# Kernel optimization log

Hardware: AMD Instinct MI355X
Metric: run time of the kernel (lower is better)

The kernel has to match this reference:

```python
import jax, jax.numpy as jnp
import numpy as np

N_NODES = 100000
N_EDGES = 640000
IN_CH, HID_CH, OUT_CH = 128, 256, 64


def setup_inputs() -> dict:
    key = jax.random.key(0)
    ks = jax.random.split(key, 6)
    x = jax.random.normal(ks[0], (N_NODES, IN_CH), dtype=jnp.float32)
    edge_index = jax.random.randint(ks[1], (2, N_EDGES), 0, N_NODES, dtype=jnp.int64)
    # Glorot-ish scaled weights
    W1l = jax.random.normal(ks[2], (HID_CH, IN_CH), dtype=jnp.float32) * (1.0 / np.sqrt(IN_CH))
    W1r = jax.random.normal(ks[3], (HID_CH, IN_CH), dtype=jnp.float32) * (1.0 / np.sqrt(IN_CH))
    W2l = jax.random.normal(ks[4], (OUT_CH, HID_CH), dtype=jnp.float32) * (1.0 / np.sqrt(HID_CH))
    W2r = jax.random.normal(ks[5], (OUT_CH, HID_CH), dtype=jnp.float32) * (1.0 / np.sqrt(HID_CH))
    b1 = jnp.zeros((HID_CH,), dtype=jnp.float32)
    b2 = jnp.zeros((OUT_CH,), dtype=jnp.float32)
    return {"x": x, "edge_index": edge_index, "W1l": W1l, "b1": b1, "W1r": W1r,
            "W2l": W2l, "b2": b2, "W2r": W2r}


def _sage_conv(x, src, dst, Wl, bl, Wr, n_nodes):
    # mean aggregation of source features at destination nodes (PyG aggr='mean')
    agg = jax.ops.segment_sum(x[src], dst, num_segments=n_nodes)          # [N, d]
    cnt = jax.ops.segment_sum(jnp.ones((src.shape[0], 1), x.dtype), dst,
                              num_segments=n_nodes)                        # [N, 1]
    mean = agg / jnp.maximum(cnt, 1.0)
    # out = lin_l(mean_neighbors) + lin_r(x); bias lives on lin_l
    return mean @ Wl.T + bl + x @ Wr.T


def reference(x, edge_index, W1l, b1, W1r, W2l, b2, W2r):
    src, dst = edge_index[0], edge_index[1]
    n = x.shape[0]
    h = _sage_conv(x, src, dst, W1l, b1, W1r, n)
    h = jax.nn.relu(h)
    out = _sage_conv(h, src, dst, W2l, b2, W2r, n)
    return out
```

## Files before the change

kernel.cpp:

```cpp
#include <hip/hip_runtime.h>


#define IN_CH  128
#define HID_CH 256
#define OUT_CH 64

typedef __bf16 bf16x8 __attribute__((ext_vector_type(8)));
typedef __bf16 bf16x4 __attribute__((ext_vector_type(4)));
typedef float  f32x4  __attribute__((ext_vector_type(4)));


__global__ void hist_kernel(const int* __restrict__ dst, int* __restrict__ deg, int E) {
    for (int e = blockIdx.x * blockDim.x + threadIdx.x; e < E; e += gridDim.x * blockDim.x)
        atomicAdd(&deg[dst[e]], 1);
}

__global__ void scan_block(const int* __restrict__ deg, int* __restrict__ offs,
                           int* __restrict__ bsum, int n) {
    __shared__ int s[512];
    int i = blockIdx.x * 512 + threadIdx.x;
    int v = (i < n) ? deg[i] : 0;
    s[threadIdx.x] = v;
    __syncthreads();
    #pragma unroll
    for (int d = 1; d < 512; d <<= 1) {
        int t = (threadIdx.x >= d) ? s[threadIdx.x - d] : 0;
        __syncthreads();
        s[threadIdx.x] += t;
        __syncthreads();
    }
    if (i < n) offs[i] = s[threadIdx.x] - v;
    if (threadIdx.x == 511) bsum[blockIdx.x] = s[511];
}

__global__ void scan_sums(int* __restrict__ bsum, int nb) {
    __shared__ int s[256];
    int v = (threadIdx.x < nb) ? bsum[threadIdx.x] : 0;
    s[threadIdx.x] = v;
    __syncthreads();
    #pragma unroll
    for (int d = 1; d < 256; d <<= 1) {
        int t = (threadIdx.x >= d) ? s[threadIdx.x - d] : 0;
        __syncthreads();
        s[threadIdx.x] += t;
        __syncthreads();
    }
    if (threadIdx.x < nb) bsum[threadIdx.x] = s[threadIdx.x] - v;
}

__global__ void scan_add(int* __restrict__ offs, const int* __restrict__ bsum, int n, int E) {
    int i = blockIdx.x * blockDim.x + threadIdx.x;
    if (i < n) offs[i] += bsum[i >> 9];
    if (i == 0) offs[n] = E;
}

__global__ void fill_csr(const int* __restrict__ src, const int* __restrict__ dst,
                         const int* __restrict__ offs, int* __restrict__ cur,
                         int* __restrict__ srcs, int E) {
    for (int e = blockIdx.x * blockDim.x + threadIdx.x; e < E; e += gridDim.x * blockDim.x) {
        int d = dst[e];
        int p = atomicAdd(&cur[d], 1);
        srcs[offs[d] + p] = src[e];
    }
}


__global__ void convert_weights(const float* __restrict__ W1l, const float* __restrict__ W1r,
                                const float* __restrict__ W2l, const float* __restrict__ W2r,
                                const float* __restrict__ b2,
                                __bf16* __restrict__ W1h, __bf16* __restrict__ W1lo,
                                __bf16* __restrict__ W2h, __bf16* __restrict__ W2lo,
                                float* __restrict__ bias2) {
    int i = blockIdx.x * 256 + threadIdx.x;
    if (i < 256 * 256) {
        int n = i >> 8, k = i & 255;
        float v = (k < 128) ? W1l[n * 128 + k] : W1r[n * 128 + (k - 128)];
        __bf16 h = (__bf16)v;
        W1h[i] = h; W1lo[i] = (__bf16)(v - (float)h);
    }
    if (i < 128 * 256) {
        int n = i >> 8, k = i & 255;
        float v = (n < 64) ? W2l[n * 256 + k] : W2r[(n - 64) * 256 + k];
        __bf16 h = (__bf16)v;
        W2h[i] = h; W2lo[i] = (__bf16)(v - (float)h);
    }
    if (i < 128) bias2[i] = (i < 64) ? 0.f : b2[i - 64];
}


__global__ __launch_bounds__(256) void agg_mean128(
    const float* __restrict__ X, const int* __restrict__ offs,
    const int* __restrict__ srcs, float* __restrict__ outm, int N) {
    int wv = (blockIdx.x * 256 + threadIdx.x) >> 6;
    int lane = threadIdx.x & 63;
    int grp = lane >> 5, l = lane & 31;
    int node = wv * 2 + grp;
    if (node >= N) return;
    int s0 = offs[node], s1 = offs[node + 1];
    float ax = 0.f, ay = 0.f, az = 0.f, aw = 0.f;
    int k = s0;
    for (; k + 4 <= s1; k += 4) {
        int i0 = srcs[k], i1 = srcs[k + 1], i2 = srcs[k + 2], i3 = srcs[k + 3];
        float4 a = *(const float4*)(X + (size_t)i0 * 128 + l * 4);
        float4 b = *(const float4*)(X + (size_t)i1 * 128 + l * 4);
        float4 c = *(const float4*)(X + (size_t)i2 * 128 + l * 4);
        float4 d = *(const float4*)(X + (size_t)i3 * 128 + l * 4);
        ax += (a.x + b.x) + (c.x + d.x);
        ay += (a.y + b.y) + (c.y + d.y);
        az += (a.z + b.z) + (c.z + d.z);
        aw += (a.w + b.w) + (c.w + d.w);
    }
    for (; k < s1; ++k) {
        int s = srcs[k];
        float4 a = *(const float4*)(X + (size_t)s * 128 + l * 4);
        ax += a.x; ay += a.y; az += a.z; aw += a.w;
    }
    int c = s1 - s0;
    float sc = 1.0f / (float)(c > 1 ? c : 1);
    float4 r; r.x = ax * sc; r.y = ay * sc; r.z = az * sc; r.w = aw * sc;
    *(float4*)(outm + (size_t)node * 128 + l * 4) = r;
}

__global__ __launch_bounds__(256) void agg_add_out(
    const float* __restrict__ Y2Z, const int* __restrict__ offs,
    const int* __restrict__ srcs, float* __restrict__ out, int N) {
    int wv = (blockIdx.x * 256 + threadIdx.x) >> 6;
    int lane = threadIdx.x & 63;
    int grp = lane >> 4, l = lane & 15;
    int node = wv * 4 + grp;
    if (node >= N) return;
    int s0 = offs[node], s1 = offs[node + 1];
    float4 z = *(const float4*)(Y2Z + (size_t)node * 128 + 64 + l * 4);
    float ax = 0.f, ay = 0.f, az = 0.f, aw = 0.f;
    int k = s0;
    for (; k + 4 <= s1; k += 4) {
        int i0 = srcs[k], i1 = srcs[k + 1], i2 = srcs[k + 2], i3 = srcs[k + 3];
        float4 a = *(const float4*)(Y2Z + (size_t)i0 * 128 + l * 4);
        float4 b = *(const float4*)(Y2Z + (size_t)i1 * 128 + l * 4);
        float4 c = *(const float4*)(Y2Z + (size_t)i2 * 128 + l * 4);
        float4 d = *(const float4*)(Y2Z + (size_t)i3 * 128 + l * 4);
        ax += (a.x + b.x) + (c.x + d.x);
        ay += (a.y + b.y) + (c.y + d.y);
        az += (a.z + b.z) + (c.z + d.z);
        aw += (a.w + b.w) + (c.w + d.w);
    }
    for (; k < s1; ++k) {
        int s = srcs[k];
        float4 a = *(const float4*)(Y2Z + (size_t)s * 128 + l * 4);
        ax += a.x; ay += a.y; az += a.z; aw += a.w;
    }
    int c = s1 - s0;
    float sc = 1.0f / (float)(c > 1 ? c : 1);
    float4 r;
    r.x = ax * sc + z.x; r.y = ay * sc + z.y;
    r.z = az * sc + z.z; r.w = aw * sc + z.w;
    *(float4*)(out + (size_t)node * 64 + l * 4) = r;
}


template<bool RELU>
__global__ __launch_bounds__(256) void gemm_split(
    const float* __restrict__ A1, int lda1,
    const float* __restrict__ A2, int lda2, int Ksplit,
    const __bf16* __restrict__ Whi, const __bf16* __restrict__ Wlo,
    const float* __restrict__ bias, float* __restrict__ C,
    int M, int K, int NT) {
    __shared__ __bf16 Ah[128 * 32], Al[128 * 32], Bh[128 * 32], Bl[128 * 32];
    const int tid = threadIdx.x;
    const int lane = tid & 63;
    const int wid = tid >> 6;
    const int wm = wid >> 1, wn = wid & 1;
    const int l15 = lane & 15, lg = lane >> 4;
    const long row0 = (long)blockIdx.x * 128;
    const int col0 = blockIdx.y * 128;

    const int ar  = tid >> 3;
    const int acx = (tid & 7) * 4;
    const int wrr = tid >> 2;
    const int wcx = (tid & 3) * 8;

    f32x4 acc[4][4] = {};

    for (int k0 = 0; k0 < K; k0 += 32) {
        const float* Asrc; int lda, kk0;
        if (k0 < Ksplit) { Asrc = A1; lda = lda1; kk0 = k0; }
        else             { Asrc = A2; lda = lda2; kk0 = k0 - Ksplit; }

        #pragma unroll
        for (int p = 0; p < 4; ++p) {
            int r = ar + p * 32;
            long gr = row0 + r;
            float4 v = make_float4(0.f, 0.f, 0.f, 0.f);
            if (gr < M) v = *(const float4*)(Asrc + gr * (long)lda + kk0 + acx);
            __bf16 h0 = (__bf16)v.x, h1 = (__bf16)v.y, h2 = (__bf16)v.z, h3 = (__bf16)v.w;
            bf16x4 hv, lv;
            hv[0] = h0; hv[1] = h1; hv[2] = h2; hv[3] = h3;
            lv[0] = (__bf16)(v.x - (float)h0); lv[1] = (__bf16)(v.y - (float)h1);
            lv[2] = (__bf16)(v.z - (float)h2); lv[3] = (__bf16)(v.w - (float)h3);
            int off = (r * 64 + acx * 2) ^ (((r >> 1) & 3) << 4);
            *(bf16x4*)((char*)Ah + off) = hv;
            *(bf16x4*)((char*)Al + off) = lv;
        }
        #pragma unroll
        for (int p = 0; p < 2; ++p) {
            int n = wrr + p * 64;
            long wrow = (long)(col0 + n) * K + k0 + wcx;
            bf16x8 hv = *(const bf16x8*)(Whi + wrow);
            bf16x8 lv = *(const bf16x8*)(Wlo + wrow);
            int off = (n * 64 + wcx * 2) ^ (((n >> 1) & 3) << 4);
            *(bf16x8*)((char*)Bh + off) = hv;
            *(bf16x8*)((char*)Bl + off) = lv;
        }
        __syncthreads();

        bf16x8 ah[4], al[4], bh[4], bl[4];
        #pragma unroll
        for (int m = 0; m < 4; ++m) {
            int r = wm * 64 + m * 16 + l15;
            int off = (r * 64 + lg * 16) ^ (((r >> 1) & 3) << 4);
            ah[m] = *(const bf16x8*)((char*)Ah + off);
            al[m] = *(const bf16x8*)((char*)Al + off);
        }
        #pragma unroll
        for (int n = 0; n < 4; ++n) {
            int r = wn * 64 + n * 16 + l15;
            int off = (r * 64 + lg * 16) ^ (((r >> 1) & 3) << 4);
            bh[n] = *(const bf16x8*)((char*)Bh + off);
            bl[n] = *(const bf16x8*)((char*)Bl + off);
        }
        #pragma unroll
        for (int m = 0; m < 4; ++m)
            #pragma unroll
            for (int n = 0; n < 4; ++n) {
                acc[m][n] = __builtin_amdgcn_mfma_f32_16x16x32_bf16(ah[m], bh[n], acc[m][n], 0, 0, 0);
                acc[m][n] = __builtin_amdgcn_mfma_f32_16x16x32_bf16(ah[m], bl[n], acc[m][n], 0, 0, 0);
                acc[m][n] = __builtin_amdgcn_mfma_f32_16x16x32_bf16(al[m], bh[n], acc[m][n], 0, 0, 0);
            }
        __syncthreads();
    }

    float bvals[4];
    #pragma unroll
    for (int n = 0; n < 4; ++n) bvals[n] = bias[col0 + wn * 64 + n * 16 + l15];
    #pragma unroll
    for (int m = 0; m < 4; ++m) {
        long gr0 = row0 + wm * 64 + m * 16 + lg * 4;
        #pragma unroll
        for (int rr = 0; rr < 4; ++rr) {
            long gr = gr0 + rr;
            if (gr < M) {
                #pragma unroll
                for (int n = 0; n < 4; ++n) {
                    int gc = col0 + wn * 64 + n * 16 + l15;
                    float v = acc[m][n][rr] + bvals[n];
                    if (RELU) v = fmaxf(v, 0.f);
                    C[gr * NT + gc] = v;
                }
            }
        }
    }
}


extern "C" void kernel_launch(void* const* d_in, const int* in_sizes, int n_in,
                              void* d_out, int out_size, void* d_ws, size_t ws_size,
                              hipStream_t stream) {
    const float* x   = (const float*)d_in[0];
    const int*   ei  = (const int*)d_in[1];
    const float* W1l = (const float*)d_in[2];
    const float* b1  = (const float*)d_in[3];
    const float* W1r = (const float*)d_in[4];
    const float* W2l = (const float*)d_in[5];
    const float* b2  = (const float*)d_in[6];
    const float* W2r = (const float*)d_in[7];
    float* out = (float*)d_out;

    const int N = in_sizes[0] / IN_CH;
    const int E = in_sizes[1] / 2;
    const int* src = ei;
    const int* dst = ei + E;

    float* h   = (float*)d_ws;
    float* buf = h + (size_t)N * HID_CH;
    int* deg  = (int*)(buf + (size_t)N * 128);
    int* offs = deg + N;
    int* cur  = offs + (N + 8);
    int* bsum = cur + N;
    int* srcs = bsum + 512;
    uintptr_t pp = (uintptr_t)(srcs + E);
    pp = (pp + 15) & ~(uintptr_t)15;
    __bf16* W1h  = (__bf16*)pp;
    __bf16* W1lo = W1h + 256 * 256;
    __bf16* W2h  = W1lo + 256 * 256;
    __bf16* W2lo = W2h + 128 * 256;
    float* bias2 = (float*)(W2lo + 128 * 256);

    hipMemsetAsync(deg, 0, sizeof(int) * N, stream);
    hipMemsetAsync(cur, 0, sizeof(int) * N, stream);

    convert_weights<<<256, 256, 0, stream>>>(W1l, W1r, W2l, W2r, b2,
                                             W1h, W1lo, W2h, W2lo, bias2);

    hist_kernel<<<1024, 256, 0, stream>>>(dst, deg, E);
    int nb = (N + 511) / 512;
    scan_block<<<nb, 512, 0, stream>>>(deg, offs, bsum, N);
    scan_sums<<<1, 256, 0, stream>>>(bsum, nb);
    scan_add<<<(N + 255) / 256, 256, 0, stream>>>(offs, bsum, N, E);
    fill_csr<<<1024, 256, 0, stream>>>(src, dst, offs, cur, srcs, E);

    agg_mean128<<<((N + 1) / 2 * 64 + 255) / 256, 256, 0, stream>>>(x, offs, srcs, buf, N);
    dim3 g1((N + 127) / 128, 2);
    gemm_split<true><<<g1, 256, 0, stream>>>(buf, IN_CH, x, IN_CH, IN_CH,
                                             W1h, W1lo, b1, h, N, 2 * IN_CH, HID_CH);

    dim3 g2((N + 127) / 128, 1);
    gemm_split<false><<<g2, 256, 0, stream>>>(nullptr, 0, h, HID_CH, 0,
                                              W2h, W2lo, bias2, buf, N, HID_CH, 2 * OUT_CH);
    agg_add_out<<<((N + 3) / 4 * 64 + 255) / 256, 256, 0, stream>>>(buf, offs, srcs, out, N);
}
```

Baseline: 376.6 us.

## Fuse layer-1 and layer-2 GEMMs keeping hidden activations in LDS

Replaces the two split-bf16 GEMM launches with one kernel that computes a 64-row tile of the layer-1 output (bias and ReLU applied), stores it as hi/lo bf16 in shared memory, and then multiplies it by the layer-2 weights. This removes the write and re-read of the N x 256 fp32 hidden tensor through global memory and drops one launch. In exchange each block uses 80 KB of LDS with 64-row tiles, which lowers occupancy and halves per-block row reuse of the weight tiles.

```diff
diff --git a/kernel.cpp b/kernel.cpp
--- a/kernel.cpp
+++ b/kernel.cpp
@@ -158,75 +158,73 @@
 }
 
 
-template<bool RELU>
-__global__ __launch_bounds__(256) void gemm_split(
-    const float* __restrict__ A1, int lda1,
-    const float* __restrict__ A2, int lda2, int Ksplit,
-    const __bf16* __restrict__ Whi, const __bf16* __restrict__ Wlo,
-    const float* __restrict__ bias, float* __restrict__ C,
-    int M, int K, int NT) {
-    __shared__ __bf16 Ah[128 * 32], Al[128 * 32], Bh[128 * 32], Bl[128 * 32];
+__global__ __launch_bounds__(256) void fused_l1l2(
+    const float* __restrict__ mean1, const float* __restrict__ x,
+    const __bf16* __restrict__ W1h, const __bf16* __restrict__ W1lo,
+    const float* __restrict__ b1,
+    const __bf16* __restrict__ W2h, const __bf16* __restrict__ W2lo,
+    const float* __restrict__ bias2,
+    float* __restrict__ Y2Z, int N) {
+    __shared__ __align__(16) char lds[80 * 1024];
+    __bf16* Hh    = (__bf16*)lds;
+    __bf16* Hl    = (__bf16*)(lds + 32 * 1024);
+    __bf16* W2hs  = (__bf16*)(lds + 64 * 1024);
+    __bf16* W2ls  = (__bf16*)(lds + 72 * 1024);
+    __bf16* Ah    = (__bf16*)lds;
+    __bf16* Al    = (__bf16*)(lds + 4 * 1024);
+    __bf16* B1h   = (__bf16*)(lds + 8 * 1024);
+    __bf16* B1l   = (__bf16*)(lds + 24 * 1024);
+
     const int tid = threadIdx.x;
     const int lane = tid & 63;
-    const int wid = tid >> 6;
-    const int wm = wid >> 1, wn = wid & 1;
+    const int w = tid >> 6;
     const int l15 = lane & 15, lg = lane >> 4;
-    const long row0 = (long)blockIdx.x * 128;
-    const int col0 = blockIdx.y * 128;
-
-    const int ar  = tid >> 3;
-    const int acx = (tid & 7) * 4;
-    const int wrr = tid >> 2;
-    const int wcx = (tid & 3) * 8;
+    const long row0 = (long)blockIdx.x * 64;
 
     f32x4 acc[4][4] = {};
-
-    for (int k0 = 0; k0 < K; k0 += 32) {
-        const float* Asrc; int lda, kk0;
-        if (k0 < Ksplit) { Asrc = A1; lda = lda1; kk0 = k0; }
-        else             { Asrc = A2; lda = lda2; kk0 = k0 - Ksplit; }
-
-        #pragma unroll
-        for (int p = 0; p < 4; ++p) {
-            int r = ar + p * 32;
+    for (int k0 = 0; k0 < 256; k0 += 32) {
+        const float* Asrc = (k0 < 128) ? mean1 : x;
+        const int kk0 = (k0 < 128) ? k0 : k0 - 128;
+        #pragma unroll
+        for (int p = 0; p < 2; ++p) {
+            int r = (tid >> 3) + p * 32;
             long gr = row0 + r;
             float4 v = make_float4(0.f, 0.f, 0.f, 0.f);
-            if (gr < M) v = *(const float4*)(Asrc + gr * (long)lda + kk0 + acx);
+            if (gr < N) v = *(const float4*)(Asrc + gr * 128 + kk0 + (tid & 7) * 4);
             __bf16 h0 = (__bf16)v.x, h1 = (__bf16)v.y, h2 = (__bf16)v.z, h3 = (__bf16)v.w;
             bf16x4 hv, lv;
             hv[0] = h0; hv[1] = h1; hv[2] = h2; hv[3] = h3;
             lv[0] = (__bf16)(v.x - (float)h0); lv[1] = (__bf16)(v.y - (float)h1);
             lv[2] = (__bf16)(v.z - (float)h2); lv[3] = (__bf16)(v.w - (float)h3);
-            int off = (r * 64 + acx * 2) ^ (((r >> 1) & 3) << 4);
+            int off = (r * 64 + (tid & 7) * 8) ^ (((r >> 1) & 3) << 4);
             *(bf16x4*)((char*)Ah + off) = hv;
             *(bf16x4*)((char*)Al + off) = lv;
         }
         #pragma unroll
-        for (int p = 0; p < 2; ++p) {
-            int n = wrr + p * 64;
-            long wrow = (long)(col0 + n) * K + k0 + wcx;
-            bf16x8 hv = *(const bf16x8*)(Whi + wrow);
-            bf16x8 lv = *(const bf16x8*)(Wlo + wrow);
-            int off = (n * 64 + wcx * 2) ^ (((n >> 1) & 3) << 4);
-            *(bf16x8*)((char*)Bh + off) = hv;
-            *(bf16x8*)((char*)Bl + off) = lv;
-        }
-        __syncthreads();
-
+        for (int p = 0; p < 4; ++p) {
+            int n = (tid >> 2) + p * 64;
+            long g = (long)n * 256 + k0 + (tid & 3) * 8;
+            bf16x8 hv = *(const bf16x8*)(W1h + g);
+            bf16x8 lv = *(const bf16x8*)(W1lo + g);
+            int off = (n * 64 + (tid & 3) * 16) ^ (((n >> 1) & 3) << 4);
+            *(bf16x8*)((char*)B1h + off) = hv;
+            *(bf16x8*)((char*)B1l + off) = lv;
+        }
+        __syncthreads();
         bf16x8 ah[4], al[4], bh[4], bl[4];
         #pragma unroll
         for (int m = 0; m < 4; ++m) {
-            int r = wm * 64 + m * 16 + l15;
+            int r = m * 16 + l15;
             int off = (r * 64 + lg * 16) ^ (((r >> 1) & 3) << 4);
             ah[m] = *(const bf16x8*)((char*)Ah + off);
             al[m] = *(const bf16x8*)((char*)Al + off);
         }
         #pragma unroll
         for (int n = 0; n < 4; ++n) {
-            int r = wn * 64 + n * 16 + l15;
-            int off = (r * 64 + lg * 16) ^ (((r >> 1) & 3) << 4);
-            bh[n] = *(const bf16x8*)((char*)Bh + off);
-            bl[n] = *(const bf16x8*)((char*)Bl + off);
+            int rb = w * 64 + n * 16 + l15;
+            int off = (rb * 64 + lg * 16) ^ (((rb >> 1) & 3) << 4);
+            bh[n] = *(const bf16x8*)((char*)B1h + off);
+            bl[n] = *(const bf16x8*)((char*)B1l + off);
         }
         #pragma unroll
         for (int m = 0; m < 4; ++m)
@@ -239,23 +237,75 @@
         __syncthreads();
     }
 
-    float bvals[4];
     #pragma unroll
-    for (int n = 0; n < 4; ++n) bvals[n] = bias[col0 + wn * 64 + n * 16 + l15];
+    for (int n = 0; n < 4; ++n) {
+        int col = w * 64 + n * 16 + l15;
+        float bv = b1[col];
+        #pragma unroll
+        for (int m = 0; m < 4; ++m) {
+            #pragma unroll
+            for (int rr = 0; rr < 4; ++rr) {
+                int row = m * 16 + lg * 4 + rr;
+                float v = fmaxf(acc[m][n][rr] + bv, 0.f);
+                __bf16 hv = (__bf16)v;
+                __bf16 lv = (__bf16)(v - (float)hv);
+                int off = (row * 512 + col * 2) ^ ((row & 7) << 4);
+                *(__bf16*)((char*)Hh + off) = hv;
+                *(__bf16*)((char*)Hl + off) = lv;
+            }
+        }
+    }
+    __syncthreads();
+
+    f32x4 acc2[4][2] = {};
+    for (int k0 = 0; k0 < 256; k0 += 32) {
+        #pragma unroll
+        for (int p = 0; p < 2; ++p) {
+            int n = (tid >> 2) + p * 64;
+            long g = (long)n * 256 + k0 + (tid & 3) * 8;
+            bf16x8 hv = *(const bf16x8*)(W2h + g);
+            bf16x8 lv = *(const bf16x8*)(W2lo + g);
+            int off = (n * 64 + (tid & 3) * 16) ^ (((n >> 1) & 3) << 4);
+            *(bf16x8*)((char*)W2hs + off) = hv;
+            *(bf16x8*)((char*)W2ls + off) = lv;
+        }
+        __syncthreads();
+        bf16x8 a2h[4], a2l[4], b2h[2], b2l[2];
+        #pragma unroll
+        for (int m = 0; m < 4; ++m) {
+            int row = m * 16 + l15;
+            int off = (row * 512 + k0 * 2 + lg * 16) ^ ((row & 7) << 4);
+            a2h[m] = *(const bf16x8*)((char*)Hh + off);
+            a2l[m] = *(const bf16x8*)((char*)Hl + off);
+        }
+        #pragma unroll
+        for (int n = 0; n < 2; ++n) {
+            int rb = w * 32 + n * 16 + l15;
+            int off = (rb * 64 + lg * 16) ^ (((rb >> 1) & 3) << 4);
+            b2h[n] = *(const bf16x8*)((char*)W2hs + off);
+            b2l[n] = *(const bf16x8*)((char*)W2ls + off);
+        }
+        #pragma unroll
+        for (int m = 0; m < 4; ++m)
+            #pragma unroll
+            for (int n = 0; n < 2; ++n) {
+                acc2[m][n] = __builtin_amdgcn_mfma_f32_16x16x32_bf16(a2h[m], b2h[n], acc2[m][n], 0, 0, 0);
+                acc2[m][n] = __builtin_amdgcn_mfma_f32_16x16x32_bf16(a2h[m], b2l[n], acc2[m][n], 0, 0, 0);
+                acc2[m][n] = __builtin_amdgcn_mfma_f32_16x16x32_bf16(a2l[m], b2h[n], acc2[m][n], 0, 0, 0);
+            }
+        __syncthreads();
+    }
+
     #pragma unroll
-    for (int m = 0; m < 4; ++m) {
-        long gr0 = row0 + wm * 64 + m * 16 + lg * 4;
-        #pragma unroll
-        for (int rr = 0; rr < 4; ++rr) {
-            long gr = gr0 + rr;
-            if (gr < M) {
-                #pragma unroll
-                for (int n = 0; n < 4; ++n) {
-                    int gc = col0 + wn * 64 + n * 16 + l15;
-                    float v = acc[m][n][rr] + bvals[n];
-                    if (RELU) v = fmaxf(v, 0.f);
-                    C[gr * NT + gc] = v;
-                }
+    for (int n = 0; n < 2; ++n) {
+        int gc = w * 32 + n * 16 + l15;
+        float bv = bias2[gc];
+        #pragma unroll
+        for (int m = 0; m < 4; ++m) {
+            #pragma unroll
+            for (int rr = 0; rr < 4; ++rr) {
+                long gr = row0 + m * 16 + lg * 4 + rr;
+                if (gr < N) Y2Z[gr * 128 + gc] = acc2[m][n][rr] + bv;
             }
         }
     }
@@ -280,9 +330,9 @@
     const int* src = ei;
     const int* dst = ei + E;
 
-    float* h   = (float*)d_ws;
-    float* buf = h + (size_t)N * HID_CH;
-    int* deg  = (int*)(buf + (size_t)N * 128);
+    float* buf1 = (float*)d_ws;
+    float* buf2 = buf1 + (size_t)N * 128;
+    int* deg  = (int*)(buf2 + (size_t)N * 128);
     int* offs = deg + N;
     int* cur  = offs + (N + 8);
     int* bsum = cur + N;
@@ -308,13 +358,10 @@
     scan_add<<<(N + 255) / 256, 256, 0, stream>>>(offs, bsum, N, E);
     fill_csr<<<1024, 256, 0, stream>>>(src, dst, offs, cur, srcs, E);
 
-    agg_mean128<<<((N + 1) / 2 * 64 + 255) / 256, 256, 0, stream>>>(x, offs, srcs, buf, N);
-    dim3 g1((N + 127) / 128, 2);
-    gemm_split<true><<<g1, 256, 0, stream>>>(buf, IN_CH, x, IN_CH, IN_CH,
-                                             W1h, W1lo, b1, h, N, 2 * IN_CH, HID_CH);
-
-    dim3 g2((N + 127) / 128, 1);
-    gemm_split<false><<<g2, 256, 0, stream>>>(nullptr, 0, h, HID_CH, 0,
-                                              W2h, W2lo, bias2, buf, N, HID_CH, 2 * OUT_CH);
-    agg_add_out<<<((N + 3) / 4 * 64 + 255) / 256, 256, 0, stream>>>(buf, offs, srcs, out, N);
-}
+    agg_mean128<<<((N + 1) / 2 * 64 + 255) / 256, 256, 0, stream>>>(x, offs, srcs, buf1, N);
+
+    fused_l1l2<<<(N + 63) / 64, 256, 0, stream>>>(buf1, x, W1h, W1lo, b1,
+                                                  W2h, W2lo, bias2, buf2, N);
+
+    agg_add_out<<<((N + 3) / 4 * 64 + 255) / 256, 256, 0, stream>>>(buf2, offs, srcs, out, N);
+}
```

Result: no change. 371.3 us (-1.4%).
